# Performance work log

Measured on AMD Instinct MI355X. Metric: run time of the kernel, lower is better.

Reference implementation:

```python
import jax, jax.numpy as jnp
import numpy as np

N_NODES = 100000
N_EDGES = 3200000
STATE_DIM = 128
ACTION_DIM = 8


def _w(key, shape, scale=0.05):
    return (jax.random.normal(key, shape, dtype=jnp.float32) * scale)


def setup_inputs() -> dict:
    key = jax.random.key(0)
    ks = jax.random.split(key, 24)
    x = jax.random.normal(ks[0], (N_NODES, STATE_DIM), dtype=jnp.float32)
    edge_index = jax.random.randint(ks[1], (2, N_EDGES), 0, N_NODES, dtype=jnp.int64)
    inp = {
        "x": x,
        "edge_index": edge_index,
        # GCN layers (weights stored [in, out] so forward is x @ W + b)
        "W1": _w(ks[2], (STATE_DIM, 128)), "b1": jnp.zeros((128,), jnp.float32),
        "W2": _w(ks[3], (128, 128)),       "b2": jnp.zeros((128,), jnp.float32),
        "W3": _w(ks[4], (128, 64)),        "b3": jnp.zeros((64,), jnp.float32),
        # actor MLP 64->128->64->ACTION_DIM + softmax
        "Wa1": _w(ks[5], (64, 128)),  "ba1": jnp.zeros((128,), jnp.float32),
        "Wa2": _w(ks[6], (128, 64)),  "ba2": jnp.zeros((64,), jnp.float32),
        "Wa3": _w(ks[7], (64, ACTION_DIM)), "ba3": jnp.zeros((ACTION_DIM,), jnp.float32),
        # critic MLP 64->128->64->1
        "Wc1": _w(ks[8], (64, 128)),  "bc1": jnp.zeros((128,), jnp.float32),
        "Wc2": _w(ks[9], (128, 64)),  "bc2": jnp.zeros((64,), jnp.float32),
        "Wc3": _w(ks[10], (64, 1)),   "bc3": jnp.zeros((1,), jnp.float32),
    }
    return inp


def _gcn_conv(x, W, b, src, dst, norm):
    # GCNConv: D^{-1/2} (A + I) D^{-1/2} X W + b  (self loops already in src/dst)
    h = x @ W                                   # [N, out]
    msg = h[src] * norm[:, None]                # gather + per-edge scale
    agg = jax.ops.segment_sum(msg, dst, num_segments=N_NODES)
    return agg + b


def reference(x, edge_index,
              W1, b1, W2, b2, W3, b3,
              Wa1, ba1, Wa2, ba2, Wa3, ba3,
              Wc1, bc1, Wc2, bc2, Wc3, bc3):
    loop = jnp.arange(N_NODES, dtype=edge_index.dtype)
    src = jnp.concatenate([edge_index[0], loop])
    dst = jnp.concatenate([edge_index[1], loop])
    deg = jax.ops.segment_sum(jnp.ones_like(dst, dtype=x.dtype), dst,
                              num_segments=N_NODES)
    dinv = jax.lax.rsqrt(deg)                   # deg >= 1 via self loops
    norm = dinv[src] * dinv[dst]                # [E+N]

    # forward_gnn (dropout is identity in eval mode)
    h = jax.nn.relu(_gcn_conv(x, W1, b1, src, dst, norm))
    h = jax.nn.relu(_gcn_conv(h, W2, b2, src, dst, norm))
    h = _gcn_conv(h, W3, b3, src, dst, norm)    # [N, 64]

    a = jax.nn.relu(h @ Wa1 + ba1)
    a = jax.nn.relu(a @ Wa2 + ba2)
    probs = jax.nn.softmax(a @ Wa3 + ba3, axis=-1)   # [N, ACTION_DIM]

    c = jax.nn.relu(h @ Wc1 + bc1)
    c = jax.nn.relu(c @ Wc2 + bc2)
    values = c @ Wc3 + bc3                      # [N, 1]

    return jnp.concatenate([probs, values], axis=-1)  # [N, ACTION_DIM+1]
```

## Files before the change

kernel.cpp:

```cpp
#include <hip/hip_runtime.h>
#include <hip/hip_bf16.h>
#include <math.h>


#define WS_ALIGN(x) (((x) + 255) & ~(size_t)255)

constexpr int RNG  = 64;
constexpr int NRG  = 1563;
constexpr int NB   = 1024;
constexpr int CHK  = 16;

constexpr float S_FP8     = 64.0f;
constexpr float S_FP8_INV = 1.0f / 64.0f;

using bf16x8 = __attribute__((ext_vector_type(8))) short;
using f32x4  = __attribute__((ext_vector_type(4))) float;
using f32x2  = __attribute__((ext_vector_type(2))) float;

__device__ __forceinline__ float b2f(unsigned short u) {
    return __uint_as_float(((unsigned int)u) << 16);
}
__device__ __forceinline__ unsigned short f2b(float f) {
    __hip_bfloat16 hb = __float2bfloat16(f);
    return *(unsigned short*)&hb;
}
__device__ __forceinline__ unsigned char f2fp8(float f) {
    return (unsigned char)(__builtin_amdgcn_cvt_pk_fp8_f32(f, f, 0, false) & 0xff);
}
__device__ __forceinline__ int pad8(int v) { return (v + 7) & ~7; }

__device__ __forceinline__ void acc8(uint2 u, f32x2& a01, f32x2& a23,
                                     f32x2& a45, f32x2& a67) {
    a01 += __builtin_amdgcn_cvt_pk_f32_fp8((int)u.x, false);
    a23 += __builtin_amdgcn_cvt_pk_f32_fp8((int)u.x, true);
    a45 += __builtin_amdgcn_cvt_pk_f32_fp8((int)u.y, false);
    a67 += __builtin_amdgcn_cvt_pk_f32_fp8((int)u.y, true);
}


__global__ __launch_bounds__(256) void bucket_count_k(
    const int* __restrict__ dst, int* __restrict__ bcnt, int E) {
    __shared__ int c64[RNG];
    int b = blockIdx.x, t = threadIdx.x;
    if (t < RNG) c64[t] = 0;
    __syncthreads();
    int ec = (E + NB - 1) / NB;
    int e0 = b * ec, e1 = min(E, e0 + ec);
    for (int e = e0 + t; e < e1; e += 256) {
        int d = __builtin_nontemporal_load(dst + e);
        atomicAdd(&c64[d / NRG], 1);
    }
    __syncthreads();
    if (t < RNG) bcnt[t * NB + b] = c64[t];
}

__global__ __launch_bounds__(256) void rsum_k(
    const int* __restrict__ bcnt, int* __restrict__ base, int* __restrict__ rtot) {
    __shared__ int s[256];
    int r = blockIdx.x, t = threadIdx.x;
    const int* row = bcnt + (size_t)r * NB;
    int v[4], loc = 0;
#pragma unroll
    for (int j = 0; j < 4; j++) { v[j] = row[t * 4 + j]; loc += v[j]; }
    s[t] = loc;
    __syncthreads();
    for (int d = 1; d < 256; d <<= 1) {
        int x = (t >= d) ? s[t - d] : 0;
        __syncthreads();
        s[t] += x;
        __syncthreads();
    }
    int run = s[t] - loc;
    int* bp = base + (size_t)r * NB + t * 4;
#pragma unroll
    for (int j = 0; j < 4; j++) { bp[j] = run; run += v[j]; }
    if (t == 255) rtot[r] = s[255];
}

__global__ void rstart_k(const int* __restrict__ rtot, int* __restrict__ bstart, int E) {
    if (threadIdx.x == 0) {
        int run = 0;
        for (int r = 0; r < RNG; r++) { bstart[r] = run; run += rtot[r]; }
        bstart[RNG] = run;
    }
}

__global__ __launch_bounds__(256) void bucket_scatter_k(
    const int* __restrict__ src, const int* __restrict__ dst,
    const int* __restrict__ base, const int* __restrict__ bstart,
    unsigned* __restrict__ bucket, int E) {
    __shared__ int cur[RNG];
    int b = blockIdx.x, t = threadIdx.x;
    if (t < RNG) cur[t] = bstart[t] + base[(size_t)t * NB + b];
    __syncthreads();
    int ec = (E + NB - 1) / NB;
    int e0 = b * ec, e1 = min(E, e0 + ec);
    for (int e = e0 + t; e < e1; e += 256) {
        int d = __builtin_nontemporal_load(dst + e);
        int sv = __builtin_nontemporal_load(src + e);
        int r = d / NRG;
        int pos = atomicAdd(&cur[r], 1);
        bucket[pos] = ((unsigned)(d - r * NRG) << 17) | (unsigned)sv;
    }
}

__global__ __launch_bounds__(256) void hist_bucket_k(
    const unsigned* __restrict__ bucket, const int* __restrict__ bstart,
    int* __restrict__ hist) {
    __shared__ int h[NRG];
    int b = blockIdx.x, r = b & 63, c2 = b >> 6, t = threadIdx.x;
    for (int i = t; i < NRG; i += 256) h[i] = 0;
    int s0 = bstart[r], s1 = bstart[r + 1];
    int ec = (s1 - s0 + CHK - 1) / CHK;
    int e0 = s0 + c2 * ec, e1 = min(s1, e0 + ec);
    __syncthreads();
    for (int e = e0 + t; e < e1; e += 256) {
        unsigned v = __builtin_nontemporal_load(bucket + e);
        atomicAdd(&h[v >> 17], 1);
    }
    __syncthreads();
    int* out = hist + ((size_t)r * CHK + c2) * NRG;
    for (int i = t; i < NRG; i += 256) out[i] = h[i];
}

__global__ void sum_hist_dinv_k(const int* __restrict__ hist, int* __restrict__ cnt,
                                float* __restrict__ dinv, int N) {
    int i = blockIdx.x * 256 + threadIdx.x;
    if (i >= N) return;
    int r = i / NRG, li = i - r * NRG;
    const int* hp = hist + ((size_t)r * CHK) * NRG + li;
    int s = 0;
#pragma unroll
    for (int c = 0; c < CHK; c++) s += hp[(size_t)c * NRG];
    cnt[i] = s;
    dinv[i] = rsqrtf((float)s + 1.0f);
}

__global__ void chunk_sum_k(const int* __restrict__ cnt, int* __restrict__ bsum, int n) {
    __shared__ int sd[256];
    int t = threadIdx.x;
    int i = blockIdx.x * 256 + t;
    sd[t] = (i < n) ? pad8(cnt[i]) : 0;
    __syncthreads();
    for (int d = 128; d > 0; d >>= 1) {
        if (t < d) sd[t] += sd[t + d];
        __syncthreads();
    }
    if (t == 0) bsum[blockIdx.x] = sd[0];
}

__global__ void scan_mid_k(const int* __restrict__ bsum, int* __restrict__ boff,
                           int nb, int* __restrict__ rowptr, int N) {
    __shared__ int s[512];
    int t = threadIdx.x;
    s[t] = (t < nb) ? bsum[t] : 0;
    __syncthreads();
    if (t == 0) {
        int run = 0;
        for (int i = 0; i < nb; i++) { int v = s[i]; s[i] = run; run += v; }
        rowptr[N] = run;
    }
    __syncthreads();
    if (t < nb) boff[t] = s[t];
}

__global__ void scan_off_pad_k(const int* __restrict__ cnt, const int* __restrict__ boff,
                               int* __restrict__ rowptr, int* __restrict__ hist,
                               int* __restrict__ col, int N) {
    __shared__ int s[256];
    int t = threadIdx.x;
    int i = blockIdx.x * 256 + t;
    int cv = (i < N) ? cnt[i] : 0;
    int v = pad8(cv);
    if (i >= N) v = 0;
    s[t] = v;
    __syncthreads();
    for (int d = 1; d < 256; d <<= 1) {
        int x = (t >= d) ? s[t - d] : 0;
        __syncthreads();
        s[t] += x;
        __syncthreads();
    }
    if (i < N) {
        int rp = s[t] - v + boff[blockIdx.x];
        rowptr[i] = rp;
        int r = i / NRG, li = i - r * NRG;
        int* hp = hist + ((size_t)r * CHK) * NRG + li;
        int run = rp;
#pragma unroll
        for (int c = 0; c < CHK; c++) {
            int hv = hp[(size_t)c * NRG];
            hp[(size_t)c * NRG] = run;
            run += hv;
        }
        for (int e = rp + cv; e < rp + v; e++) col[e] = N;
    }
}

__global__ __launch_bounds__(256) void fill2_k(
    const unsigned* __restrict__ bucket, const int* __restrict__ bstart,
    const int* __restrict__ hist, int* __restrict__ col) {
    __shared__ int cur[NRG];
    int b = blockIdx.x, r = b & 63, c2 = b >> 6, t = threadIdx.x;
    const int* hp = hist + ((size_t)r * CHK + c2) * NRG;
    for (int i = t; i < NRG; i += 256) cur[i] = hp[i];
    int s0 = bstart[r], s1 = bstart[r + 1];
    int ec = (s1 - s0 + CHK - 1) / CHK;
    int e0 = s0 + c2 * ec, e1 = min(s1, e0 + ec);
    __syncthreads();
    for (int e = e0 + t; e < e1; e += 256) {
        unsigned v = __builtin_nontemporal_load(bucket + e);
        int slot = atomicAdd(&cur[v >> 17], 1);
        col[slot] = (int)(v & 0x1FFFFu);
    }
}


__global__ __launch_bounds__(256) void prep_w_k(
    const float* __restrict__ W1, const float* __restrict__ W2,
    const float* __restrict__ W3, const float* __restrict__ Wa1,
    const float* __restrict__ Wc1, const float* __restrict__ Wa2,
    const float* __restrict__ Wc2, unsigned short* __restrict__ wt) {
    int i = blockIdx.x * 256 + threadIdx.x;
    const float* W; int off, K, OUT;
    if (i < 16384)      { W = W1;  off = 0;     K = 128; OUT = 128; }
    else if (i < 32768) { W = W2;  off = 16384; K = 128; OUT = 128; }
    else if (i < 40960) { W = W3;  off = 32768; K = 128; OUT = 64; }
    else if (i < 49152) { W = Wa1; off = 40960; K = 64;  OUT = 128; }
    else if (i < 57344) { W = Wc1; off = 49152; K = 64;  OUT = 128; }
    else if (i < 65536) { W = Wa2; off = 57344; K = 128; OUT = 64; }
    else                { W = Wc2; off = 65536; K = 128; OUT = 64; }
    int j = i - off, k = j / OUT, n = j - k * OUT;
    wt[off + n * K + k] = f2b(W[j]);
}


template <int K, int OUT, int EPI, bool AF32>
__global__ __launch_bounds__(256) void gemm2_k(
    const void* __restrict__ Xv, int ldx, const unsigned short* __restrict__ Wt,
    const float* __restrict__ sb, const float* __restrict__ w3b,
    const float* __restrict__ b3, void* __restrict__ Yv, int N, int NT) {
    constexpr int LDK = K + 8;
    __shared__ __align__(16) unsigned short Bs[OUT * LDK];
    __shared__ __align__(16) unsigned short As[64 * LDK];
    int t = threadIdx.x;

    for (int g = t; g < OUT * (K / 8); g += 256) {
        int r = g / (K / 8), q = g - r * (K / 8);
        *(uint4*)&Bs[r * LDK + q * 8] = *(const uint4*)(Wt + r * K + q * 8);
    }

    int wv = t >> 6, lane = t & 63;
    int lm = lane & 15, lq = lane >> 4;
    constexpr int CT = OUT / 16;

    for (int tile = blockIdx.x; tile < NT; tile += gridDim.x) {
        int rowBase = tile * 64;

        if constexpr (AF32) {
            const float* X = (const float*)Xv;
            for (int g = t; g < 64 * (K / 8); g += 256) {
                int r = g / (K / 8), q = g - r * (K / 8);
                int gr = rowBase + r;
                unsigned short us[8];
                if (gr < N) {
                    float4 v0 = *(const float4*)(X + (size_t)gr * ldx + q * 8);
                    float4 v1 = *(const float4*)(X + (size_t)gr * ldx + q * 8 + 4);
                    us[0] = f2b(v0.x); us[1] = f2b(v0.y); us[2] = f2b(v0.z); us[3] = f2b(v0.w);
                    us[4] = f2b(v1.x); us[5] = f2b(v1.y); us[6] = f2b(v1.z); us[7] = f2b(v1.w);
                } else {
#pragma unroll
                    for (int j = 0; j < 8; j++) us[j] = 0;
                }
                *(uint4*)&As[r * LDK + q * 8] = *(uint4*)us;
            }
        } else {
            const unsigned short* X = (const unsigned short*)Xv;
            for (int g = t; g < 64 * (K / 8); g += 256) {
                int r = g / (K / 8), q = g - r * (K / 8);
                int gr = rowBase + r;
                uint4 v = make_uint4(0, 0, 0, 0);
                if (gr < N) v = *(const uint4*)(X + (size_t)gr * ldx + q * 8);
                *(uint4*)&As[r * LDK + q * 8] = v;
            }
        }
        __syncthreads();

        f32x4 acc[CT];
#pragma unroll
        for (int c = 0; c < CT; c++) acc[c] = (f32x4){0.f, 0.f, 0.f, 0.f};

        const unsigned short* arow = &As[(wv * 16 + lm) * LDK + lq * 8];
#pragma unroll
        for (int kt = 0; kt < K / 32; kt++) {
            bf16x8 a = *(const bf16x8*)(arow + kt * 32);
#pragma unroll
            for (int c = 0; c < CT; c++) {
                bf16x8 b = *(const bf16x8*)&Bs[(c * 16 + lm) * LDK + kt * 32 + lq * 8];
                acc[c] = __builtin_amdgcn_mfma_f32_16x16x32_bf16(a, b, acc[c], 0, 0, 0);
            }
        }

        int r0 = rowBase + wv * 16 + lq * 4;
        if constexpr (EPI == 0) {
#pragma unroll
            for (int r = 0; r < 4; r++) {
                int gr = r0 + r;
                float scale = (gr < N) ? sb[gr] * S_FP8 : 0.f;
#pragma unroll
                for (int c = 0; c < CT; c++) {
                    int colg = c * 16 + lm;
                    ((unsigned char*)Yv)[(size_t)gr * OUT + colg] = f2fp8(acc[c][r] * scale);
                }
            }
        } else if constexpr (EPI == 1) {
#pragma unroll
            for (int r = 0; r < 4; r++) {
                int gr = r0 + r;
                if (gr < N) {
#pragma unroll
                    for (int c = 0; c < CT; c++) {
                        int colg = c * 16 + lm;
                        float bb = (colg < 128) ? sb[colg] : w3b[colg - 128];
                        float v = fmaxf(acc[c][r] + bb, 0.f);
                        ((unsigned short*)Yv)[(size_t)gr * OUT + colg] = f2b(v);
                    }
                }
            }
        } else if constexpr (EPI == 2) {
            float l[4][8];
#pragma unroll
            for (int r = 0; r < 4; r++)
#pragma unroll
                for (int a = 0; a < 8; a++) l[r][a] = 0.f;
#pragma unroll
            for (int c = 0; c < CT; c++) {
                int colg = c * 16 + lm;
#pragma unroll
                for (int r = 0; r < 4; r++) {
                    float v = fmaxf(acc[c][r] + sb[colg], 0.f);
#pragma unroll
                    for (int a = 0; a < 8; a++)
                        l[r][a] = fmaf(v, w3b[colg * 8 + a], l[r][a]);
                }
            }
#pragma unroll
            for (int w = 1; w < 16; w <<= 1)
#pragma unroll
                for (int r = 0; r < 4; r++)
#pragma unroll
                    for (int a = 0; a < 8; a++)
                        l[r][a] += __shfl_xor(l[r][a], w, 64);
            if (lm < 8) {
#pragma unroll
                for (int r = 0; r < 4; r++) {
                    int gr = r0 + r;
                    if (gr < N) {
                        float lg[8], m = -1e30f;
#pragma unroll
                        for (int a = 0; a < 8; a++) { lg[a] = l[r][a] + b3[a]; m = fmaxf(m, lg[a]); }
                        float sum = 0.f;
#pragma unroll
                        for (int a = 0; a < 8; a++) { lg[a] = expf(lg[a] - m); sum += lg[a]; }
                        ((float*)Yv)[(size_t)gr * 9 + lm] = lg[lm] / sum;
                    }
                }
            }
        } else {
            float lv[4] = {0.f, 0.f, 0.f, 0.f};
#pragma unroll
            for (int c = 0; c < CT; c++) {
                int colg = c * 16 + lm;
#pragma unroll
                for (int r = 0; r < 4; r++) {
                    float v = fmaxf(acc[c][r] + sb[colg], 0.f);
                    lv[r] = fmaf(v, w3b[colg], lv[r]);
                }
            }
#pragma unroll
            for (int w = 1; w < 16; w <<= 1)
#pragma unroll
                for (int r = 0; r < 4; r++) lv[r] += __shfl_xor(lv[r], w, 64);
            if (lm == 0) {
#pragma unroll
                for (int r = 0; r < 4; r++) {
                    int gr = r0 + r;
                    if (gr < N) ((float*)Yv)[(size_t)gr * 9 + 8] = lv[r] + b3[0];
                }
            }
        }
        __syncthreads();
    }
}


template <bool RELU>
__global__ __launch_bounds__(256) void agg128_k(
    const unsigned char* __restrict__ H,
    const int* __restrict__ rowptr, const int* __restrict__ col,
    const float* __restrict__ dinv, const float* __restrict__ bias,
    unsigned short* __restrict__ Y, int N, int Ecap) {
    int tid = threadIdx.x;
    int node = blockIdx.x * 4 + (tid >> 6);
    if (node >= N) return;
    int lane = tid & 63;
    int grp = lane >> 4;
    int li8 = (lane & 15) * 8;

    f32x2 a01 = {0.f, 0.f}, a23 = {0.f, 0.f}, a45 = {0.f, 0.f}, a67 = {0.f, 0.f};
    if (grp == 0) {
        uint2 u = *(const uint2*)(H + (size_t)node * 128 + li8);
        acc8(u, a01, a23, a45, a67);
    }

    int start = rowptr[node], end = rowptr[node + 1];
    for (int e0 = start; e0 < end; e0 += 64) {
        int cv = col[min(e0 + lane, Ecap - 1)];
        int quads = min(64, end - e0) >> 2;
        for (int q = 0; q < quads; q += 2) {
            int s0 = __shfl(cv, 4 * q + grp, 64);
            int s1 = __shfl(cv, 4 * q + 4 + grp, 64);
            uint2 u0 = *(const uint2*)(H + (size_t)s0 * 128 + li8);
            uint2 u1 = *(const uint2*)(H + (size_t)s1 * 128 + li8);
            acc8(u0, a01, a23, a45, a67);
            acc8(u1, a01, a23, a45, a67);
        }
    }

#pragma unroll
    for (int w = 16; w < 64; w <<= 1) {
        a01[0] += __shfl_xor(a01[0], w, 64); a01[1] += __shfl_xor(a01[1], w, 64);
        a23[0] += __shfl_xor(a23[0], w, 64); a23[1] += __shfl_xor(a23[1], w, 64);
        a45[0] += __shfl_xor(a45[0], w, 64); a45[1] += __shfl_xor(a45[1], w, 64);
        a67[0] += __shfl_xor(a67[0], w, 64); a67[1] += __shfl_xor(a67[1], w, 64);
    }

    if (grp == 0) {
        float dv = dinv[node] * S_FP8_INV;
        float4 b0 = *(const float4*)(bias + li8);
        float4 b1 = *(const float4*)(bias + li8 + 4);
        float o0 = a01[0] * dv + b0.x, o1 = a01[1] * dv + b0.y;
        float o2 = a23[0] * dv + b0.z, o3 = a23[1] * dv + b0.w;
        float o4 = a45[0] * dv + b1.x, o5 = a45[1] * dv + b1.y;
        float o6 = a67[0] * dv + b1.z, o7 = a67[1] * dv + b1.w;
        if (RELU) {
            o0 = fmaxf(o0, 0.f); o1 = fmaxf(o1, 0.f); o2 = fmaxf(o2, 0.f); o3 = fmaxf(o3, 0.f);
            o4 = fmaxf(o4, 0.f); o5 = fmaxf(o5, 0.f); o6 = fmaxf(o6, 0.f); o7 = fmaxf(o7, 0.f);
        }
        unsigned short us[8] = {f2b(o0), f2b(o1), f2b(o2), f2b(o3),
                                f2b(o4), f2b(o5), f2b(o6), f2b(o7)};
        *(uint4*)(Y + (size_t)node * 128 + li8) = *(uint4*)us;
    }
}

__global__ __launch_bounds__(256) void agg64_k(
    const unsigned char* __restrict__ H,
    const int* __restrict__ rowptr, const int* __restrict__ col,
    const float* __restrict__ dinv, const float* __restrict__ bias,
    unsigned short* __restrict__ Y, int N, int Ecap) {
    int tid = threadIdx.x;
    int node = blockIdx.x * 4 + (tid >> 6);
    if (node >= N) return;
    int lane = tid & 63;
    int grp = lane >> 3;
    int li8 = (lane & 7) * 8;

    f32x2 a01 = {0.f, 0.f}, a23 = {0.f, 0.f}, a45 = {0.f, 0.f}, a67 = {0.f, 0.f};
    if (grp == 0) {
        uint2 u = *(const uint2*)(H + (size_t)node * 64 + li8);
        acc8(u, a01, a23, a45, a67);
    }

    int start = rowptr[node], end = rowptr[node + 1];
    for (int e0 = start; e0 < end; e0 += 64) {
        int cv = col[min(e0 + lane, Ecap - 1)];
        int octs = min(64, end - e0) >> 3;
        int o = 0;
        for (; o + 2 <= octs; o += 2) {
            int s0 = __shfl(cv, 8 * o + grp, 64);
            int s1 = __shfl(cv, 8 * o + 8 + grp, 64);
            uint2 u0 = *(const uint2*)(H + (size_t)s0 * 64 + li8);
            uint2 u1 = *(const uint2*)(H + (size_t)s1 * 64 + li8);
            acc8(u0, a01, a23, a45, a67);
            acc8(u1, a01, a23, a45, a67);
        }
        if (o < octs) {
            int s0 = __shfl(cv, 8 * o + grp, 64);
            uint2 u0 = *(const uint2*)(H + (size_t)s0 * 64 + li8);
            acc8(u0, a01, a23, a45, a67);
        }
    }

#pragma unroll
    for (int w = 8; w < 64; w <<= 1) {
        a01[0] += __shfl_xor(a01[0], w, 64); a01[1] += __shfl_xor(a01[1], w, 64);
        a23[0] += __shfl_xor(a23[0], w, 64); a23[1] += __shfl_xor(a23[1], w, 64);
        a45[0] += __shfl_xor(a45[0], w, 64); a45[1] += __shfl_xor(a45[1], w, 64);
        a67[0] += __shfl_xor(a67[0], w, 64); a67[1] += __shfl_xor(a67[1], w, 64);
    }

    if (grp == 0) {
        float dv = dinv[node] * S_FP8_INV;
        float4 b0 = *(const float4*)(bias + li8);
        float4 b1 = *(const float4*)(bias + li8 + 4);
        unsigned short us[8] = {
            f2b(a01[0] * dv + b0.x), f2b(a01[1] * dv + b0.y),
            f2b(a23[0] * dv + b0.z), f2b(a23[1] * dv + b0.w),
            f2b(a45[0] * dv + b1.x), f2b(a45[1] * dv + b1.y),
            f2b(a67[0] * dv + b1.z), f2b(a67[1] * dv + b1.w)};
        *(uint4*)(Y + (size_t)node * 64 + li8) = *(uint4*)us;
    }
}


extern "C" void kernel_launch(void* const* d_in, const int* in_sizes, int n_in,
                              void* d_out, int out_size, void* d_ws, size_t ws_size,
                              hipStream_t stream) {
    const float* x   = (const float*)d_in[0];
    const int*   ei  = (const int*)d_in[1];
    const float* W1  = (const float*)d_in[2];  const float* b1  = (const float*)d_in[3];
    const float* W2  = (const float*)d_in[4];  const float* b2  = (const float*)d_in[5];
    const float* W3  = (const float*)d_in[6];  const float* b3  = (const float*)d_in[7];
    const float* Wa1 = (const float*)d_in[8];  const float* ba1 = (const float*)d_in[9];
    const float* Wa2 = (const float*)d_in[10]; const float* ba2 = (const float*)d_in[11];
    const float* Wa3 = (const float*)d_in[12]; const float* ba3 = (const float*)d_in[13];
    const float* Wc1 = (const float*)d_in[14]; const float* bc1 = (const float*)d_in[15];
    const float* Wc2 = (const float*)d_in[16]; const float* bc2 = (const float*)d_in[17];
    const float* Wc3 = (const float*)d_in[18]; const float* bc3 = (const float*)d_in[19];
    float* out = (float*)d_out;

    const int N = in_sizes[0] / 128;
    const int E = in_sizes[1] / 2;
    const int* src = ei;
    const int* dst = ei + E;
    const int Ecap = E + 8 * N;
    const int Npad = ((N + 63) / 64) * 64;
    const int NT   = (N + 63) / 64;

    size_t off = 0;
    auto take = [&](size_t bytes) { size_t o = off; off = WS_ALIGN(off + bytes); return o; };
    char* ws = (char*)d_ws;
    unsigned short* h3     = (unsigned short*)(ws + take((size_t)N * 64 * 2));
    unsigned short* h      = (unsigned short*)(ws + take((size_t)N * 128 * 2));
    unsigned char*  hpr8   = (unsigned char*) (ws + take((size_t)(Npad + 64) * 128));
    int*            col    = (int*)(ws + take((size_t)Ecap * 4));
    unsigned short* wt     = (unsigned short*)(ws + take(73728 * 2));
    float* dinv   = (float*)(ws + take((size_t)(N + 64) * 4));
    int*   cnt    = (int*)  (ws + take((size_t)N * 4));
    int*   rowptr = (int*)  (ws + take((size_t)(N + 1) * 4));
    int*   bcnt   = (int*)  (ws + take((size_t)RNG * NB * 4));
    int*   base   = (int*)  (ws + take((size_t)RNG * NB * 4));
    int*   rtot   = (int*)  (ws + take(RNG * 4));
    int*   bstart = (int*)  (ws + take((RNG + 1) * 4));
    int*   bsum   = (int*)  (ws + take(512 * 4));
    int*   boff   = (int*)  (ws + take(512 * 4));
    unsigned* bucket = (unsigned*)h;
    int* hist = (int*)h3;
    unsigned short* A1C1 = (unsigned short*)h;
    (void)ws_size; (void)n_in; (void)out_size;

    const int nb  = (N + 255) / 256;
    const int gN  = (N + 255) / 256;
    const int GG  = 512;

    prep_w_k<<<288, 256, 0, stream>>>(W1, W2, W3, Wa1, Wc1, Wa2, Wc2, wt);
    const unsigned short* W1t  = wt;
    const unsigned short* W2t  = wt + 16384;
    const unsigned short* W3t  = wt + 32768;
    const unsigned short* Wh1t = wt + 40960;
    const unsigned short* Wa2t = wt + 57344;
    const unsigned short* Wc2t = wt + 65536;

    bucket_count_k<<<NB, 256, 0, stream>>>(dst, bcnt, E);
    rsum_k<<<RNG, 256, 0, stream>>>(bcnt, base, rtot);
    rstart_k<<<1, 64, 0, stream>>>(rtot, bstart, E);
    bucket_scatter_k<<<NB, 256, 0, stream>>>(src, dst, base, bstart, bucket, E);
    hist_bucket_k<<<RNG * CHK, 256, 0, stream>>>(bucket, bstart, hist);
    sum_hist_dinv_k<<<gN, 256, 0, stream>>>(hist, cnt, dinv, N);
    chunk_sum_k<<<nb, 256, 0, stream>>>(cnt, bsum, N);
    scan_mid_k<<<1, 512, 0, stream>>>(bsum, boff, nb, rowptr, N);
    scan_off_pad_k<<<nb, 256, 0, stream>>>(cnt, boff, rowptr, hist, col, N);
    fill2_k<<<RNG * CHK, 256, 0, stream>>>(bucket, bstart, hist, col);

    gemm2_k<128, 128, 0, true><<<GG, 256, 0, stream>>>(
        x, 128, W1t, dinv, nullptr, nullptr, hpr8, N, NT);
    agg128_k<true><<<(N + 3) / 4, 256, 0, stream>>>(hpr8, rowptr, col, dinv, b1, h, N, Ecap);
    gemm2_k<128, 128, 0, false><<<GG, 256, 0, stream>>>(
        h, 128, W2t, dinv, nullptr, nullptr, hpr8, N, NT);
    agg128_k<true><<<(N + 3) / 4, 256, 0, stream>>>(hpr8, rowptr, col, dinv, b2, h, N, Ecap);
    gemm2_k<128, 64, 0, false><<<GG, 256, 0, stream>>>(
        h, 128, W3t, dinv, nullptr, nullptr, hpr8, N, NT);
    agg64_k<<<(N + 3) / 4, 256, 0, stream>>>(hpr8, rowptr, col, dinv, b3, h3, N, Ecap);

    gemm2_k<64, 256, 1, false><<<GG, 256, 0, stream>>>(
        h3, 64, Wh1t, ba1, bc1, nullptr, A1C1, N, NT);
    gemm2_k<128, 64, 2, false><<<GG, 256, 0, stream>>>(
        A1C1, 256, Wa2t, ba2, Wa3, ba3, out, N, NT);
    gemm2_k<128, 64, 3, false><<<GG, 256, 0, stream>>>(
        A1C1 + 128, 256, Wc2t, bc2, Wc3, bc3, out, N, NT);
}
```

Measured before the change: 503.8 us.

## Fuse aggregation with the following GEMM and fuse each MLP head into one kernel

After: 592.9 us. 17.7% more time.

```diff
diff --git a/kernel.cpp b/kernel.cpp
--- a/kernel.cpp
+++ b/kernel.cpp
@@ -313,35 +313,204 @@
                     ((unsigned char*)Yv)[(size_t)gr * OUT + colg] = f2fp8(acc[c][r] * scale);
                 }
             }
-        } else if constexpr (EPI == 1) {
+        }
+        __syncthreads();
+    }
+}
+
+
+template <int OUT>
+__global__ __launch_bounds__(256, 8) void agg_gemm_k(
+    const unsigned char* __restrict__ H,
+    const int* __restrict__ rowptr, const int* __restrict__ col,
+    const float* __restrict__ dinv, const float* __restrict__ bias,
+    const unsigned short* __restrict__ Wt,
+    unsigned char* __restrict__ Y,
+    int N, int Ecap, int NT16) {
+    constexpr int K = 128, LDK = K + 8;
+    __shared__ __align__(16) unsigned short As[4 * 16 * LDK];
+    int t = threadIdx.x, wv = t >> 6, lane = t & 63;
+    unsigned short* Aw = &As[wv * 16 * LDK];
+    int lm = lane & 15, lq = lane >> 4;
+    int grp = lq, li8 = lm * 8;
+    int stride = gridDim.x << 2;
+
+    for (int tile = blockIdx.x * 4 + wv; tile < NT16; tile += stride) {
+        int base = tile * 16;
+
+        for (int i = 0; i < 16; i++) {
+            int node = base + i;
+            if (node < N) {
+                f32x2 a01 = {0.f, 0.f}, a23 = {0.f, 0.f}, a45 = {0.f, 0.f}, a67 = {0.f, 0.f};
+                if (grp == 0) {
+                    uint2 u = *(const uint2*)(H + (size_t)node * 128 + li8);
+                    acc8(u, a01, a23, a45, a67);
+                }
+                int start = rowptr[node], end = rowptr[node + 1];
+                for (int e0 = start; e0 < end; e0 += 64) {
+                    int cv = col[min(e0 + lane, Ecap - 1)];
+                    int quads = min(64, end - e0) >> 2;
+                    for (int q = 0; q < quads; q += 2) {
+                        int s0 = __shfl(cv, 4 * q + grp, 64);
+                        int s1 = __shfl(cv, 4 * q + 4 + grp, 64);
+                        uint2 u0 = *(const uint2*)(H + (size_t)s0 * 128 + li8);
+                        uint2 u1 = *(const uint2*)(H + (size_t)s1 * 128 + li8);
+                        acc8(u0, a01, a23, a45, a67);
+                        acc8(u1, a01, a23, a45, a67);
+                    }
+                }
+#pragma unroll
+                for (int w = 16; w < 64; w <<= 1) {
+                    a01[0] += __shfl_xor(a01[0], w, 64); a01[1] += __shfl_xor(a01[1], w, 64);
+                    a23[0] += __shfl_xor(a23[0], w, 64); a23[1] += __shfl_xor(a23[1], w, 64);
+                    a45[0] += __shfl_xor(a45[0], w, 64); a45[1] += __shfl_xor(a45[1], w, 64);
+                    a67[0] += __shfl_xor(a67[0], w, 64); a67[1] += __shfl_xor(a67[1], w, 64);
+                }
+                if (grp == 0) {
+                    float dv = dinv[node] * S_FP8_INV;
+                    float4 b0 = *(const float4*)(bias + li8);
+                    float4 b1 = *(const float4*)(bias + li8 + 4);
+                    float o0 = fmaxf(a01[0] * dv + b0.x, 0.f), o1 = fmaxf(a01[1] * dv + b0.y, 0.f);
+                    float o2 = fmaxf(a23[0] * dv + b0.z, 0.f), o3 = fmaxf(a23[1] * dv + b0.w, 0.f);
+                    float o4 = fmaxf(a45[0] * dv + b1.x, 0.f), o5 = fmaxf(a45[1] * dv + b1.y, 0.f);
+                    float o6 = fmaxf(a67[0] * dv + b1.z, 0.f), o7 = fmaxf(a67[1] * dv + b1.w, 0.f);
+                    unsigned short us[8] = {f2b(o0), f2b(o1), f2b(o2), f2b(o3),
+                                            f2b(o4), f2b(o5), f2b(o6), f2b(o7)};
+                    *(uint4*)&Aw[i * LDK + li8] = *(uint4*)us;
+                }
+            } else if (grp == 0) {
+                uint4 z = make_uint4(0, 0, 0, 0);
+                *(uint4*)&Aw[i * LDK + li8] = z;
+            }
+        }
+
+        const unsigned short* arow = &Aw[lm * LDK + lq * 8];
+#pragma unroll
+        for (int c0 = 0; c0 < OUT / 16; c0 += 4) {
+            f32x4 acc[4];
+#pragma unroll
+            for (int c = 0; c < 4; c++) acc[c] = (f32x4){0.f, 0.f, 0.f, 0.f};
+#pragma unroll
+            for (int kt = 0; kt < 4; kt++) {
+                bf16x8 a = *(const bf16x8*)(arow + kt * 32);
+#pragma unroll
+                for (int c = 0; c < 4; c++) {
+                    bf16x8 b = *(const bf16x8*)(Wt + (size_t)((c0 + c) * 16 + lm) * K + kt * 32 + lq * 8);
+                    acc[c] = __builtin_amdgcn_mfma_f32_16x16x32_bf16(a, b, acc[c], 0, 0, 0);
+                }
+            }
+            int r0 = base + lq * 4;
 #pragma unroll
             for (int r = 0; r < 4; r++) {
                 int gr = r0 + r;
-                if (gr < N) {
-#pragma unroll
-                    for (int c = 0; c < CT; c++) {
-                        int colg = c * 16 + lm;
-                        float bb = (colg < 128) ? sb[colg] : w3b[colg - 128];
-                        float v = fmaxf(acc[c][r] + bb, 0.f);
-                        ((unsigned short*)Yv)[(size_t)gr * OUT + colg] = f2b(v);
-                    }
-                }
-            }
-        } else if constexpr (EPI == 2) {
+                float scale = (gr < N) ? dinv[gr] * S_FP8 : 0.f;
+#pragma unroll
+                for (int c = 0; c < 4; c++) {
+                    int colg = (c0 + c) * 16 + lm;
+                    Y[(size_t)gr * OUT + colg] = f2fp8(acc[c][r] * scale);
+                }
+            }
+        }
+    }
+}
+
+
+template <int EPI>
+__global__ __launch_bounds__(256) void heads_k(
+    const unsigned short* __restrict__ h3,
+    const unsigned short* __restrict__ W1t,
+    const float* __restrict__ b1v,
+    const unsigned short* __restrict__ W2t,
+    const float* __restrict__ b2v,
+    const float* __restrict__ w3,
+    const float* __restrict__ b3v,
+    float* __restrict__ out, int N, int NT) {
+    constexpr int LD64 = 72, LD128 = 136;
+    __shared__ __align__(16) unsigned short Bs1[128 * LD64];
+    __shared__ __align__(16) unsigned short Bs2[64 * LD128];
+    __shared__ __align__(16) unsigned short As[4 * 16 * LD64];
+    __shared__ __align__(16) unsigned short A1[4 * 16 * LD128];
+    int t = threadIdx.x, wv = t >> 6, lane = t & 63;
+    int lm = lane & 15, lq = lane >> 4;
+
+    for (int g = t; g < 128 * 8; g += 256) {
+        int r = g >> 3, q = g & 7;
+        *(uint4*)&Bs1[r * LD64 + q * 8] = *(const uint4*)(W1t + r * 64 + q * 8);
+    }
+    for (int g = t; g < 64 * 16; g += 256) {
+        int r = g >> 4, q = g & 15;
+        *(uint4*)&Bs2[r * LD128 + q * 8] = *(const uint4*)(W2t + r * 128 + q * 8);
+    }
+    __syncthreads();
+
+    unsigned short* Asw = &As[wv * 16 * LD64];
+    unsigned short* A1w = &A1[wv * 16 * LD128];
+
+    for (int tile = blockIdx.x; tile < NT; tile += gridDim.x) {
+        int rowBase = tile * 64 + wv * 16;
+
+        for (int g = lane; g < 16 * 8; g += 64) {
+            int r = g >> 3, q = g & 7;
+            int gr = rowBase + r;
+            uint4 v = make_uint4(0, 0, 0, 0);
+            if (gr < N) v = *(const uint4*)(h3 + (size_t)gr * 64 + q * 8);
+            *(uint4*)&Asw[r * LD64 + q * 8] = v;
+        }
+
+        f32x4 acc1[8];
+#pragma unroll
+        for (int c = 0; c < 8; c++) acc1[c] = (f32x4){0.f, 0.f, 0.f, 0.f};
+        const unsigned short* arow = &Asw[lm * LD64 + lq * 8];
+#pragma unroll
+        for (int kt = 0; kt < 2; kt++) {
+            bf16x8 a = *(const bf16x8*)(arow + kt * 32);
+#pragma unroll
+            for (int c = 0; c < 8; c++) {
+                bf16x8 b = *(const bf16x8*)&Bs1[(c * 16 + lm) * LD64 + kt * 32 + lq * 8];
+                acc1[c] = __builtin_amdgcn_mfma_f32_16x16x32_bf16(a, b, acc1[c], 0, 0, 0);
+            }
+        }
+#pragma unroll
+        for (int r = 0; r < 4; r++) {
+            int lr = lq * 4 + r;
+#pragma unroll
+            for (int c = 0; c < 8; c++) {
+                int colg = c * 16 + lm;
+                float v = fmaxf(acc1[c][r] + b1v[colg], 0.f);
+                A1w[lr * LD128 + colg] = f2b(v);
+            }
+        }
+
+        f32x4 acc[4];
+#pragma unroll
+        for (int c = 0; c < 4; c++) acc[c] = (f32x4){0.f, 0.f, 0.f, 0.f};
+        const unsigned short* arow2 = &A1w[lm * LD128 + lq * 8];
+#pragma unroll
+        for (int kt = 0; kt < 4; kt++) {
+            bf16x8 a = *(const bf16x8*)(arow2 + kt * 32);
+#pragma unroll
+            for (int c = 0; c < 4; c++) {
+                bf16x8 b = *(const bf16x8*)&Bs2[(c * 16 + lm) * LD128 + kt * 32 + lq * 8];
+                acc[c] = __builtin_amdgcn_mfma_f32_16x16x32_bf16(a, b, acc[c], 0, 0, 0);
+            }
+        }
+
+        int r0 = rowBase + lq * 4;
+        if constexpr (EPI == 2) {
             float l[4][8];
 #pragma unroll
             for (int r = 0; r < 4; r++)
 #pragma unroll
                 for (int a = 0; a < 8; a++) l[r][a] = 0.f;
 #pragma unroll
-            for (int c = 0; c < CT; c++) {
+            for (int c = 0; c < 4; c++) {
                 int colg = c * 16 + lm;
 #pragma unroll
                 for (int r = 0; r < 4; r++) {
-                    float v = fmaxf(acc[c][r] + sb[colg], 0.f);
+                    float v = fmaxf(acc[c][r] + b2v[colg], 0.f);
 #pragma unroll
                     for (int a = 0; a < 8; a++)
-                        l[r][a] = fmaf(v, w3b[colg * 8 + a], l[r][a]);
+                        l[r][a] = fmaf(v, w3[colg * 8 + a], l[r][a]);
                 }
             }
 #pragma unroll
@@ -358,23 +527,23 @@
                     if (gr < N) {
                         float lg[8], m = -1e30f;
 #pragma unroll
-                        for (int a = 0; a < 8; a++) { lg[a] = l[r][a] + b3[a]; m = fmaxf(m, lg[a]); }
+                        for (int a = 0; a < 8; a++) { lg[a] = l[r][a] + b3v[a]; m = fmaxf(m, lg[a]); }
                         float sum = 0.f;
 #pragma unroll
                         for (int a = 0; a < 8; a++) { lg[a] = expf(lg[a] - m); sum += lg[a]; }
-                        ((float*)Yv)[(size_t)gr * 9 + lm] = lg[lm] / sum;
+                        out[(size_t)gr * 9 + lm] = lg[lm] / sum;
                     }
                 }
             }
         } else {
             float lv[4] = {0.f, 0.f, 0.f, 0.f};
 #pragma unroll
-            for (int c = 0; c < CT; c++) {
+            for (int c = 0; c < 4; c++) {
                 int colg = c * 16 + lm;
 #pragma unroll
                 for (int r = 0; r < 4; r++) {
-                    float v = fmaxf(acc[c][r] + sb[colg], 0.f);
-                    lv[r] = fmaf(v, w3b[colg], lv[r]);
+                    float v = fmaxf(acc[c][r] + b2v[colg], 0.f);
+                    lv[r] = fmaf(v, w3[colg], lv[r]);
                 }
             }
 #pragma unroll
@@ -385,73 +554,13 @@
 #pragma unroll
                 for (int r = 0; r < 4; r++) {
                     int gr = r0 + r;
-                    if (gr < N) ((float*)Yv)[(size_t)gr * 9 + 8] = lv[r] + b3[0];
-                }
-            }
-        }
-        __syncthreads();
-    }
-}
-
-
-template <bool RELU>
-__global__ __launch_bounds__(256) void agg128_k(
-    const unsigned char* __restrict__ H,
-    const int* __restrict__ rowptr, const int* __restrict__ col,
-    const float* __restrict__ dinv, const float* __restrict__ bias,
-    unsigned short* __restrict__ Y, int N, int Ecap) {
-    int tid = threadIdx.x;
-    int node = blockIdx.x * 4 + (tid >> 6);
-    if (node >= N) return;
-    int lane = tid & 63;
-    int grp = lane >> 4;
-    int li8 = (lane & 15) * 8;
-
-    f32x2 a01 = {0.f, 0.f}, a23 = {0.f, 0.f}, a45 = {0.f, 0.f}, a67 = {0.f, 0.f};
-    if (grp == 0) {
-        uint2 u = *(const uint2*)(H + (size_t)node * 128 + li8);
-        acc8(u, a01, a23, a45, a67);
-    }
-
-    int start = rowptr[node], end = rowptr[node + 1];
-    for (int e0 = start; e0 < end; e0 += 64) {
-        int cv = col[min(e0 + lane, Ecap - 1)];
-        int quads = min(64, end - e0) >> 2;
-        for (int q = 0; q < quads; q += 2) {
-            int s0 = __shfl(cv, 4 * q + grp, 64);
-            int s1 = __shfl(cv, 4 * q + 4 + grp, 64);
-            uint2 u0 = *(const uint2*)(H + (size_t)s0 * 128 + li8);
-            uint2 u1 = *(const uint2*)(H + (size_t)s1 * 128 + li8);
-            acc8(u0, a01, a23, a45, a67);
-            acc8(u1, a01, a23, a45, a67);
-        }
-    }
-
-#pragma unroll
-    for (int w = 16; w < 64; w <<= 1) {
-        a01[0] += __shfl_xor(a01[0], w, 64); a01[1] += __shfl_xor(a01[1], w, 64);
-        a23[0] += __shfl_xor(a23[0], w, 64); a23[1] += __shfl_xor(a23[1], w, 64);
-        a45[0] += __shfl_xor(a45[0], w, 64); a45[1] += __shfl_xor(a45[1], w, 64);
-        a67[0] += __shfl_xor(a67[0], w, 64); a67[1] += __shfl_xor(a67[1], w, 64);
-    }
-
-    if (grp == 0) {
-        float dv = dinv[node] * S_FP8_INV;
-        float4 b0 = *(const float4*)(bias + li8);
-        float4 b1 = *(const float4*)(bias + li8 + 4);
-        float o0 = a01[0] * dv + b0.x, o1 = a01[1] * dv + b0.y;
-        float o2 = a23[0] * dv + b0.z, o3 = a23[1] * dv + b0.w;
-        float o4 = a45[0] * dv + b1.x, o5 = a45[1] * dv + b1.y;
-        float o6 = a67[0] * dv + b1.z, o7 = a67[1] * dv + b1.w;
-        if (RELU) {
-            o0 = fmaxf(o0, 0.f); o1 = fmaxf(o1, 0.f); o2 = fmaxf(o2, 0.f); o3 = fmaxf(o3, 0.f);
-            o4 = fmaxf(o4, 0.f); o5 = fmaxf(o5, 0.f); o6 = fmaxf(o6, 0.f); o7 = fmaxf(o7, 0.f);
-        }
-        unsigned short us[8] = {f2b(o0), f2b(o1), f2b(o2), f2b(o3),
-                                f2b(o4), f2b(o5), f2b(o6), f2b(o7)};
-        *(uint4*)(Y + (size_t)node * 128 + li8) = *(uint4*)us;
-    }
-}
+                    if (gr < N) out[(size_t)gr * 9 + 8] = lv[r] + b3v[0];
+                }
+            }
+        }
+    }
+}
+
 
 __global__ __launch_bounds__(256) void agg64_k(
     const unsigned char* __restrict__ H,
@@ -536,6 +645,7 @@
     const int Ecap = E + 8 * N;
     const int Npad = ((N + 63) / 64) * 64;
     const int NT   = (N + 63) / 64;
+    const int NT16 = Npad / 16;
 
     size_t off = 0;
     auto take = [&](size_t bytes) { size_t o = off; off = WS_ALIGN(off + bytes); return o; };
@@ -556,7 +666,7 @@
     int*   boff   = (int*)  (ws + take(512 * 4));
     unsigned* bucket = (unsigned*)h;
     int* hist = (int*)h3;
-    unsigned short* A1C1 = (unsigned short*)h;
+    unsigned char* hpr8B = (unsigned char*)h;
     (void)ws_size; (void)n_in; (void)out_size;
 
     const int nb  = (N + 255) / 256;
@@ -584,18 +694,12 @@
 
     gemm2_k<128, 128, 0, true><<<GG, 256, 0, stream>>>(
         x, 128, W1t, dinv, nullptr, nullptr, hpr8, N, NT);
-    agg128_k<true><<<(N + 3) / 4, 256, 0, stream>>>(hpr8, rowptr, col, dinv, b1, h, N, Ecap);
-    gemm2_k<128, 128, 0, false><<<GG, 256, 0, stream>>>(
-        h, 128, W2t, dinv, nullptr, nullptr, hpr8, N, NT);
-    agg128_k<true><<<(N + 3) / 4, 256, 0, stream>>>(hpr8, rowptr, col, dinv, b2, h, N, Ecap);
-    gemm2_k<128, 64, 0, false><<<GG, 256, 0, stream>>>(
-        h, 128, W3t, dinv, nullptr, nullptr, hpr8, N, NT);
+    agg_gemm_k<128><<<2048, 256, 0, stream>>>(
+        hpr8, rowptr, col, dinv, b1, W2t, hpr8B, N, Ecap, NT16);
+    agg_gemm_k<64><<<2048, 256, 0, stream>>>(
+        hpr8B, rowptr, col, dinv, b2, W3t, hpr8, N, Ecap, NT16);
     agg64_k<<<(N + 3) / 4, 256, 0, stream>>>(hpr8, rowptr, col, dinv, b3, h3, N, Ecap);
 
-    gemm2_k<64, 256, 1, false><<<GG, 256, 0, stream>>>(
-        h3, 64, Wh1t, ba1, bc1, nullptr, A1C1, N, NT);
-    gemm2_k<128, 64, 2, false><<<GG, 256, 0, stream>>>(
-        A1C1, 256, Wa2t, ba2, Wa3, ba3, out, N, NT);
-    gemm2_k<128, 64, 3, false><<<GG, 256, 0, stream>>>(
-        A1C1 + 128, 256, Wc2t, bc2, Wc3, bc3, out, N, NT);
-}
+    heads_k<2><<<GG, 256, 0, stream>>>(h3, Wh1t, ba1, Wa2t, ba2, Wa3, ba3, out, N, NT);
+    heads_k<3><<<GG, 256, 0, stream>>>(h3, Wh1t + 128 * 64, bc1, Wc2t, bc2, Wc3, bc3, out, N, NT);
+}
```
